# Kernel optimization log

Hardware: AMD Instinct MI355X
Metric: run time of the kernel (lower is better)

The kernel has to match this reference:

```python
import jax, jax.numpy as jnp
import numpy as np

DIM = 768
HEADS = 12
HEAD_DIM = DIM // HEADS
SCALE = HEAD_DIM ** -0.5


def setup_inputs() -> dict:
    key = jax.random.key(0)
    k1, k2, k3, k4, k5 = jax.random.split(key, 5)
    B, N = 4, 2048
    x = jax.random.normal(k1, (B, N, DIM), dtype=jnp.float32)
    # qkv Linear: weight [3*dim, dim], bias [3*dim]
    w_qkv = jax.random.normal(k2, (3 * DIM, DIM), dtype=jnp.float32) * (DIM ** -0.5)
    b_qkv = jax.random.normal(k3, (3 * DIM,), dtype=jnp.float32) * 0.01
    # proj Linear: weight [dim, dim], bias [dim]
    w_proj = jax.random.normal(k4, (DIM, DIM), dtype=jnp.float32) * (DIM ** -0.5)
    b_proj = jax.random.normal(k5, (DIM,), dtype=jnp.float32) * 0.01
    return {"x": x, "w_qkv": w_qkv, "b_qkv": b_qkv, "w_proj": w_proj, "b_proj": b_proj}


def reference(x, w_qkv, b_qkv, w_proj, b_proj):
    B, N, C = x.shape
    qkv = (jnp.einsum('bnc,oc->bno', x, w_qkv) + b_qkv)
    qkv = qkv.reshape(B, N, 3, HEADS, HEAD_DIM).transpose(2, 0, 3, 1, 4)
    q, k, v = qkv[0], qkv[1], qkv[2]
    attn = jnp.einsum('bhqd,bhkd->bhqk', q, k) * SCALE
    attn = jax.nn.softmax(attn, axis=-1)
    out = jnp.einsum('bhqk,bhkd->bhqd', attn, v)  # [B, H, N, Dh]
    out = out.transpose(0, 2, 1, 3).reshape(B, N, C)
    # dropout is identity in eval mode
    return jnp.einsum('bnc,oc->bno', out, w_proj) + b_proj
```

## Files before the change

### kernel.cpp

```cpp
#include <hip/hip_runtime.h>
#include <hip/hip_bf16.h>

using bf16 = __hip_bfloat16;
typedef __bf16 bf16x8 __attribute__((ext_vector_type(8)));
typedef short short4v __attribute__((ext_vector_type(4)));
typedef short short8v __attribute__((ext_vector_type(8)));
typedef float float4v __attribute__((ext_vector_type(4)));

#define DIM   768
#define NH    12
#define HD    64
#define SEQ   2048
#define BATCH 4
#define TOK   (BATCH * SEQ)
#define SCALE_QL2E 0.18033688011112042f

#define NX  (TOK * DIM)
#define NWQ (3 * DIM * DIM)
#define NWP (DIM * DIM)

__device__ __forceinline__ short f2bf(float f) {
  union { bf16 h; short s; } u;
  u.h = __float2bfloat16(f);
  return u.s;
}

union frag8 { short4v h[2]; short8v s; bf16x8 b; };

__device__ __forceinline__ void async_copy16(const bf16* g, short* l) {
  __builtin_amdgcn_global_load_lds(
      (const __attribute__((address_space(1))) unsigned int*)g,
      (__attribute__((address_space(3))) unsigned int*)l, 16, 0, 0);
}
__device__ __forceinline__ void async_copy4(const bf16* g, short* l) {
  __builtin_amdgcn_global_load_lds(
      (const __attribute__((address_space(1))) unsigned int*)g,
      (__attribute__((address_space(3))) unsigned int*)l, 4, 0, 0);
}

__global__ void __launch_bounds__(256)
cvt3(const float* __restrict__ a, bf16* __restrict__ oa, long na,
     const float* __restrict__ b, bf16* __restrict__ ob, long nb,
     const float* __restrict__ c, bf16* __restrict__ oc, long nc) {
  const long i = ((long)blockIdx.x * 256 + threadIdx.x) * 8;
  const float* src; bf16* dst; long off;
  if (i < na)                { src = a; dst = oa; off = i; }
  else if (i < na + nb)      { src = b; dst = ob; off = i - na; }
  else if (i < na + nb + nc) { src = c; dst = oc; off = i - na - nb; }
  else return;
  const float4v x0 = *(const float4v*)(src + off);
  const float4v x1 = *(const float4v*)(src + off + 4);
  short8v r;
  r[0] = f2bf(x0[0]); r[1] = f2bf(x0[1]); r[2] = f2bf(x0[2]); r[3] = f2bf(x0[3]);
  r[4] = f2bf(x1[0]); r[5] = f2bf(x1[1]); r[6] = f2bf(x1[2]); r[7] = f2bf(x1[3]);
  *(short8v*)(dst + off) = r;
}

__device__ __forceinline__ void gemm_mainloop(const bf16* __restrict__ A,
                                              const bf16* __restrict__ B,
                                              short* As, short* Bs,
                                              float4v acc[4][4]) {
  const int t = threadIdx.x;
  const int w = t >> 6, l = t & 63, lr = l & 15, q = l >> 4;
  const int wr = ((w >> 1) << 6), wc = ((w & 1) << 6);

  const bf16* Ag = A + (t >> 2) * DIM + (t & 3) * 8;
  const bf16* Bg = B + (t >> 2) * DIM + (t & 3) * 8;

  for (int k0 = 0; k0 < DIM; k0 += 32) {
    __syncthreads();
    async_copy16(Ag,            &As[t * 8]);
    async_copy16(Ag + 64 * DIM, &As[2048 + t * 8]);
    async_copy16(Bg,            &Bs[t * 8]);
    async_copy16(Bg + 64 * DIM, &Bs[2048 + t * 8]);
    Ag += 32; Bg += 32;
    __syncthreads();

    bf16x8 af[4], bfv[4];
#pragma unroll
    for (int i = 0; i < 4; ++i)
      af[i] = *(const bf16x8*)&As[(wr + i * 16 + lr) * 32 + q * 8];
#pragma unroll
    for (int j = 0; j < 4; ++j)
      bfv[j] = *(const bf16x8*)&Bs[(wc + j * 16 + lr) * 32 + q * 8];
#pragma unroll
    for (int i = 0; i < 4; ++i)
#pragma unroll
      for (int j = 0; j < 4; ++j)
        acc[i][j] = __builtin_amdgcn_mfma_f32_16x16x32_bf16(af[i], bfv[j],
                                                            acc[i][j], 0, 0, 0);
  }
}

#define VW0 asm volatile("s_waitcnt vmcnt(0)" ::: "memory")
#define BARRIER __builtin_amdgcn_s_barrier()
#define LGKM0 asm volatile("s_waitcnt lgkmcnt(0)" ::: "memory")
#define NOSTG (void)0
#define NOVW  (void)0

#define STGP(s, p)                                                            \
  async_copy16(pa + (p) * 32,             &As[s][t * 8]);                     \
  async_copy16(pa + 64 * DIM + (p) * 32,  &As[s][2048 + t * 8]);              \
  async_copy16(pb + (p) * 32,             &Bs[s][t * 8]);                     \
  async_copy16(pb + 64 * DIM + (p) * 32,  &Bs[s][2048 + t * 8]);              \
  async_copy16(pb + 128 * DIM + (p) * 32, &Bs[s][4096 + t * 8]);              \
  async_copy16(pb + 192 * DIM + (p) * 32, &Bs[s][6144 + t * 8]);              \
  async_copy4 (pb3 + (p) * 32,            &Bs[s][8192 + t * 2]);              \
  async_copy4 (pb3 + 16 * DIM + (p) * 32, &Bs[s][8704 + t * 2])

#define PHASE(CUR, STG_, VW_) {                                               \
  bf16x8 af[4], bfv[9];                                                       \
  _Pragma("unroll") for (int mf_ = 0; mf_ < 4; ++mf_)                         \
    af[mf_] = *(const bf16x8*)&As[CUR][mf_ * 512 + arow];                     \
  _Pragma("unroll") for (int nf_ = 0; nf_ < 9; ++nf_)                         \
    bfv[nf_] = *(const bf16x8*)&Bs[CUR][nf_ * 512 + brow];                    \
  STG_; BARRIER; LGKM0;                                                       \
  __builtin_amdgcn_s_setprio(1);                                              \
  _Pragma("unroll") for (int mf_ = 0; mf_ < 4; ++mf_)                         \
  _Pragma("unroll") for (int nf_ = 0; nf_ < 9; ++nf_)                         \
    acc[mf_][nf_] = __builtin_amdgcn_mfma_f32_16x16x32_bf16(                  \
        af[mf_], bfv[nf_], acc[mf_][nf_], 0, 0, 0);                           \
  __builtin_amdgcn_s_setprio(0); VW_; BARRIER; }

__global__ void __launch_bounds__(256, 2)
gemm_qkv(const bf16* __restrict__ X, const bf16* __restrict__ W,
         const float* __restrict__ bias,
         bf16* __restrict__ qb, bf16* __restrict__ kb, bf16* __restrict__ vb) {
  __shared__ short As[2][128 * 32];
  __shared__ short Bs[2][288 * 32];
  const int t = threadIdx.x;
  const int w = t >> 6, l = t & 63, lr = l & 15, q = l >> 4;
  const int wm = w >> 1, wn = w & 1;

  const int orig = blockIdx.x;
  const int swz = (orig & 7) * 64 + (orig >> 3);
  const int tm = swz >> 3, tn = swz & 7;
  const int row0 = tm * 128, col0 = tn * 288;

  const int sr = t >> 2;
  const int scol = (((t & 3) << 3) ^ (((sr >> 1) & 3) << 3));
  const bf16* pa  = X + (size_t)(row0 + sr) * DIM + scol;
  const bf16* pb  = W + (size_t)(col0 + sr) * DIM + scol;
  const int r3 = t >> 4;
  const int c3 = ((t & 15) << 1) ^ (((r3 >> 1) & 3) << 3);
  const bf16* pb3 = W + (size_t)(col0 + 256 + r3) * DIM + c3;

  const int acol = ((q << 3) ^ (((lr >> 1) & 3) << 3));
  const int arow = (wm * 64 + lr) * 32 + acol;
  const int brow = (wn * 144 + lr) * 32 + acol;

  float4v acc[4][9] = {};

  STGP(0, 0);
  VW0; BARRIER;

#pragma unroll 1
  for (int k = 0; k < 22; k += 2) {
    PHASE(0, STGP(1, k + 1), VW0)
    PHASE(1, STGP(0, k + 2), VW0)
  }
  PHASE(0, STGP(1, 23), VW0)
  PHASE(1, NOSTG,       NOVW)

#pragma unroll
  for (int nf = 0; nf < 9; ++nf) {
    const int gn = col0 + wn * 144 + nf * 16 + lr;
    const int which = gn / DIM;
    const int cc = gn - which * DIM;
    const int hh = cc >> 6, dd = cc & 63;
    const float bv = bias[gn];
#pragma unroll
    for (int mf = 0; mf < 4; ++mf) {
      const int gm0 = row0 + wm * 64 + mf * 16 + (q << 2);
      const int b = gm0 >> 11, n0 = gm0 & 2047;
      if (which == 2) {
        short4v pv;
#pragma unroll
        for (int r = 0; r < 4; ++r) pv[r] = f2bf(acc[mf][nf][r] + bv);
        *(short4v*)&vb[((size_t)(b * NH + hh) * HD + dd) * SEQ + n0] = pv;
      } else {
        bf16* dst = (which == 0) ? qb : kb;
        const float sc = (which == 0) ? SCALE_QL2E : 1.0f;
#pragma unroll
        for (int r = 0; r < 4; ++r)
          dst[((size_t)(b * NH + hh) * SEQ + n0 + r) * HD + dd] =
              __float2bfloat16((acc[mf][nf][r] + bv) * sc);
      }
    }
  }
}

__global__ void __launch_bounds__(256, 3)
flash_attn(const bf16* __restrict__ Qp, const bf16* __restrict__ Kp,
           const bf16* __restrict__ Vtp, bf16* __restrict__ Op) {
  const int bh = blockIdx.y, qt = blockIdx.x;
  const int t = threadIdx.x, w = t >> 6, l = t & 63, lr = l & 15, q = l >> 4;
  __shared__ short Ks[2][64 * 68];
  __shared__ short Vt[2][64 * 66];

  const bf16* Qb = Qp  + (size_t)(bh * SEQ + qt * 128) * HD;
  const bf16* Kb = Kp  + (size_t)bh * SEQ * HD;
  const bf16* Vb = Vtp + (size_t)bh * HD * SEQ;

  const int tr3 = t >> 3, td8 = (t & 7) * 8;

#pragma unroll
  for (int i = 0; i < 4; ++i) {
    const int row = i * 32 + tr3;
    *(short8v*)&Ks[row >> 6][(row & 63) * 68 + td8] =
        *(const short8v*)(Qb + (size_t)row * HD + td8);
  }
  __syncthreads();
  bf16x8 qf[2][2];
#pragma unroll
  for (int it = 0; it < 2; ++it)
#pragma unroll
    for (int kq = 0; kq < 2; ++kq) {
      const int row = w * 32 + it * 16 + lr;
      qf[it][kq] = *(const bf16x8*)&Ks[row >> 6][(row & 63) * 68 + kq * 32 + q * 8];
    }
  __syncthreads();

  short8v kr[2], vr[2];
#pragma unroll
  for (int i = 0; i < 2; ++i) {
    kr[i] = *(const short8v*)(Kb + (size_t)(i * 32 + tr3) * HD + td8);
    vr[i] = *(const short8v*)(Vb + (size_t)(i * 32 + tr3) * SEQ + td8);
  }

  frag8 ones;
#pragma unroll
  for (int r = 0; r < 8; ++r) ones.s[r] = (short)0x3F80;

  float4v o[2][4] = {};
  float4v lacc[2] = {};

  for (int kt = 0; kt < 32; ++kt) {
    const int cur = kt & 1;
#pragma unroll
    for (int i = 0; i < 2; ++i) {
      *(short8v*)&Ks[cur][(i * 32 + tr3) * 68 + td8] = kr[i];
      *(short8v*)&Vt[cur][(i * 32 + tr3) * 66 + td8] = vr[i];
    }
    if (kt < 31) {
      const int k1 = (kt + 1) * 64;
#pragma unroll
      for (int i = 0; i < 2; ++i) {
        kr[i] = *(const short8v*)(Kb + (size_t)(k1 + i * 32 + tr3) * HD + td8);
        vr[i] = *(const short8v*)(Vb + (size_t)(i * 32 + tr3) * SEQ + k1 + td8);
      }
    }
    __syncthreads();

    float4v s[4][2] = {};
    __builtin_amdgcn_s_setprio(1);
#pragma unroll
    for (int jn = 0; jn < 4; ++jn) {
      bf16x8 kf[2];
#pragma unroll
      for (int kq = 0; kq < 2; ++kq)
        kf[kq] = *(const bf16x8*)&Ks[cur][(jn * 16 + lr) * 68 + kq * 32 + q * 8];
#pragma unroll
      for (int it = 0; it < 2; ++it)
#pragma unroll
        for (int kq = 0; kq < 2; ++kq)
          s[jn][it] = __builtin_amdgcn_mfma_f32_16x16x32_bf16(kf[kq], qf[it][kq],
                                                              s[jn][it], 0, 0, 0);
    }
    __builtin_amdgcn_s_setprio(0);

    frag8 pf[2][2];
#pragma unroll
    for (int it = 0; it < 2; ++it)
#pragma unroll
      for (int c4 = 0; c4 < 2; ++c4)
#pragma unroll
        for (int r = 0; r < 4; ++r) {
          pf[c4][it].s[r]     = f2bf(__builtin_amdgcn_exp2f(s[2 * c4][it][r]));
          pf[c4][it].s[4 + r] = f2bf(__builtin_amdgcn_exp2f(s[2 * c4 + 1][it][r]));
        }

    __builtin_amdgcn_s_setprio(1);
#pragma unroll
    for (int c4 = 0; c4 < 2; ++c4) {
#pragma unroll
      for (int dj = 0; dj < 4; ++dj) {
        frag8 vf;
        vf.h[0] = *(const short4v*)&Vt[cur][(dj * 16 + lr) * 66 + c4 * 32 + (q << 2)];
        vf.h[1] = *(const short4v*)&Vt[cur][(dj * 16 + lr) * 66 + c4 * 32 + 16 + (q << 2)];
#pragma unroll
        for (int it = 0; it < 2; ++it)
          o[it][dj] = __builtin_amdgcn_mfma_f32_16x16x32_bf16(pf[c4][it].b, vf.b,
                                                              o[it][dj], 0, 0, 0);
      }
#pragma unroll
      for (int it = 0; it < 2; ++it)
        lacc[it] = __builtin_amdgcn_mfma_f32_16x16x32_bf16(pf[c4][it].b, ones.b,
                                                           lacc[it], 0, 0, 0);
    }
    __builtin_amdgcn_s_setprio(0);
  }

  const int b = bh / NH, h = bh - b * NH;
#pragma unroll
  for (int it = 0; it < 2; ++it)
#pragma unroll
    for (int r = 0; r < 4; ++r) {
      const float linv = 1.0f / lacc[it][r];
      const int grow = b * SEQ + qt * 128 + w * 32 + it * 16 + (q << 2) + r;
      bf16* orow = Op + (size_t)grow * DIM + h * HD;
#pragma unroll
      for (int dj = 0; dj < 4; ++dj)
        orow[dj * 16 + lr] = __float2bfloat16(o[it][dj][r] * linv);
    }
}

__global__ void __launch_bounds__(256)
gemm_proj(const bf16* __restrict__ A, const bf16* __restrict__ W,
          const float* __restrict__ bias, float* __restrict__ out) {
  __shared__ short As[128 * 32];
  __shared__ short Bs[128 * 32];
  const int t = threadIdx.x;
  const int w = t >> 6, l = t & 63, lr = l & 15, q = l >> 4;
  const int wr = ((w >> 1) << 6), wc = ((w & 1) << 6);
  const int row0 = blockIdx.y * 128, col0 = blockIdx.x * 128;

  float4v acc[4][4] = {};
  gemm_mainloop(A + row0 * DIM, W + col0 * DIM, As, Bs, acc);

#pragma unroll
  for (int j = 0; j < 4; ++j) {
    const int gn = col0 + wc + j * 16 + lr;
    const float bv = bias[gn];
#pragma unroll
    for (int i = 0; i < 4; ++i) {
#pragma unroll
      for (int r = 0; r < 4; ++r) {
        const int gm = row0 + wr + i * 16 + (q << 2) + r;
        out[(size_t)gm * DIM + gn] = acc[i][j][r] + bv;
      }
    }
  }
}

extern "C" void kernel_launch(void* const* d_in, const int* in_sizes, int n_in,
                              void* d_out, int out_size, void* d_ws, size_t ws_size,
                              hipStream_t stream) {
  const float* x      = (const float*)d_in[0];
  const float* w_qkv  = (const float*)d_in[1];
  const float* b_qkv  = (const float*)d_in[2];
  const float* w_proj = (const float*)d_in[3];
  const float* b_proj = (const float*)d_in[4];
  float* out = (float*)d_out;

  const size_t perbuf = (size_t)BATCH * NH * SEQ * HD;
  bf16* qb  = (bf16*)d_ws;
  bf16* kb  = qb + perbuf;
  bf16* vb  = kb + perbuf;
  bf16* ao  = vb + perbuf;
  bf16* xb  = ao + perbuf;
  bf16* wqb = xb + (size_t)NX;
  bf16* wpb = wqb + (size_t)NWQ;

  const int cvt_blocks = (NX + NWQ + NWP) / 8 / 256;
  cvt3<<<cvt_blocks, 256, 0, stream>>>(x, xb, NX, w_qkv, wqb, NWQ, w_proj, wpb, NWP);
  gemm_qkv <<<dim3(512), 256, 0, stream>>>(xb, wqb, b_qkv, qb, kb, vb);
  flash_attn<<<dim3(SEQ / 128, BATCH * NH), 256, 0, stream>>>(qb, kb, vb, ao);
  gemm_proj <<<dim3(DIM / 128, TOK / 128),  256, 0, stream>>>(ao, wpb, b_proj, out);
}
```

Baseline: 205.8 us.

## Enlarge QKV GEMM tile to 256x288 with 8 waves and split-quadrant pipelined staging

Rewrites the QKV projection GEMM to use 512-thread blocks, each computing a 256x288 output tile with a K-step of 64. Operand tiles are split into four shared-memory sub-buffers, and global-to-LDS copies for the next tile are interleaved between the four quadrant MFMA sub-phases, with partial vmcnt waits so loads stay in flight. The larger tile increases operand reuse and halves the grid to 256 blocks, at the cost of much more LDS per block, more barriers, and fewer blocks, which may hurt occupancy and the tail on the device.

```diff
diff --git a/kernel.cpp b/kernel.cpp
--- a/kernel.cpp
+++ b/kernel.cpp
@@ -92,86 +92,128 @@
   }
 }
 
+#define VW8 asm volatile("s_waitcnt vmcnt(8)" ::: "memory")
 #define VW0 asm volatile("s_waitcnt vmcnt(0)" ::: "memory")
 #define BARRIER __builtin_amdgcn_s_barrier()
 #define LGKM0 asm volatile("s_waitcnt lgkmcnt(0)" ::: "memory")
 #define NOSTG (void)0
 #define NOVW  (void)0
 
-#define STGP(s, p)                                                            \
-  async_copy16(pa + (p) * 32,             &As[s][t * 8]);                     \
-  async_copy16(pa + 64 * DIM + (p) * 32,  &As[s][2048 + t * 8]);              \
-  async_copy16(pb + (p) * 32,             &Bs[s][t * 8]);                     \
-  async_copy16(pb + 64 * DIM + (p) * 32,  &Bs[s][2048 + t * 8]);              \
-  async_copy16(pb + 128 * DIM + (p) * 32, &Bs[s][4096 + t * 8]);              \
-  async_copy16(pb + 192 * DIM + (p) * 32, &Bs[s][6144 + t * 8]);              \
-  async_copy4 (pb3 + (p) * 32,            &Bs[s][8192 + t * 2]);              \
-  async_copy4 (pb3 + 16 * DIM + (p) * 32, &Bs[s][8704 + t * 2])
-
-#define PHASE(CUR, STG_, VW_) {                                               \
-  bf16x8 af[4], bfv[9];                                                       \
-  _Pragma("unroll") for (int mf_ = 0; mf_ < 4; ++mf_)                         \
-    af[mf_] = *(const bf16x8*)&As[CUR][mf_ * 512 + arow];                     \
-  _Pragma("unroll") for (int nf_ = 0; nf_ < 9; ++nf_)                         \
-    bfv[nf_] = *(const bf16x8*)&Bs[CUR][nf_ * 512 + brow];                    \
-  STG_; BARRIER; LGKM0;                                                       \
+#define STG_A0(c, k) { async_copy16(pa    + (k),      &As0[c][t * 8]);        \
+                       async_copy16(pa    + (k) + 32, &As0[c][4096 + t * 8]); }
+#define STG_A1(c, k) { async_copy16(pa128 + (k),      &As1[c][t * 8]);        \
+                       async_copy16(pa128 + (k) + 32, &As1[c][4096 + t * 8]); }
+#define STG_B0(c, k) { async_copy16(pw0   + (k),      &Bs0[c][t * 8]);        \
+                       async_copy16(pw0   + (k) + 32, &Bs0[c][4096 + t * 8]); }
+#define STG_B1(c, k) { async_copy16(pw128 + (k),      &Bs1[c][t * 8]);        \
+                       async_copy4 (pw256 + (k),      &Bs1[c][4096 + t * 2]); \
+                       async_copy16(pw128 + (k) + 32, &Bs1[c][5120 + t * 8]); \
+                       async_copy4 (pw256 + (k) + 32, &Bs1[c][9216 + t * 2]); }
+
+#define KTILE(C, ST1, ST2, ST3, ST4, VW_) {                                   \
+  bf16x8 a0[2][2], a1[2][2], b0[4][2], b1[5][2];                              \
+  _Pragma("unroll") for (int m_ = 0; m_ < 2; ++m_) {                          \
+    a0[m_][0] = *(const bf16x8*)&As0[C][m_ * 2048 + arow];                    \
+    a0[m_][1] = *(const bf16x8*)&As0[C][4096 + m_ * 2048 + arow]; }           \
+  _Pragma("unroll") for (int n_ = 0; n_ < 4; ++n_) {                          \
+    b0[n_][0] = *(const bf16x8*)&Bs0[C][n_ * 1024 + brow];                    \
+    b0[n_][1] = *(const bf16x8*)&Bs0[C][4096 + n_ * 1024 + brow]; }           \
+  ST1; BARRIER; LGKM0;                                                        \
   __builtin_amdgcn_s_setprio(1);                                              \
-  _Pragma("unroll") for (int mf_ = 0; mf_ < 4; ++mf_)                         \
-  _Pragma("unroll") for (int nf_ = 0; nf_ < 9; ++nf_)                         \
-    acc[mf_][nf_] = __builtin_amdgcn_mfma_f32_16x16x32_bf16(                  \
-        af[mf_], bfv[nf_], acc[mf_][nf_], 0, 0, 0);                           \
+  _Pragma("unroll") for (int m_ = 0; m_ < 2; ++m_)                            \
+  _Pragma("unroll") for (int n_ = 0; n_ < 4; ++n_)                            \
+  _Pragma("unroll") for (int p_ = 0; p_ < 2; ++p_)                            \
+    acc[m_][n_] = __builtin_amdgcn_mfma_f32_16x16x32_bf16(                    \
+        a0[m_][p_], b0[n_][p_], acc[m_][n_], 0, 0, 0);                        \
+  __builtin_amdgcn_s_setprio(0); BARRIER;                                     \
+  _Pragma("unroll") for (int m_ = 0; m_ < 2; ++m_) {                          \
+    a1[m_][0] = *(const bf16x8*)&As1[C][m_ * 2048 + arow];                    \
+    a1[m_][1] = *(const bf16x8*)&As1[C][4096 + m_ * 2048 + arow]; }           \
+  ST2; BARRIER; LGKM0;                                                        \
+  __builtin_amdgcn_s_setprio(1);                                              \
+  _Pragma("unroll") for (int m_ = 0; m_ < 2; ++m_)                            \
+  _Pragma("unroll") for (int n_ = 0; n_ < 4; ++n_)                            \
+  _Pragma("unroll") for (int p_ = 0; p_ < 2; ++p_)                            \
+    acc[2 + m_][n_] = __builtin_amdgcn_mfma_f32_16x16x32_bf16(                \
+        a1[m_][p_], b0[n_][p_], acc[2 + m_][n_], 0, 0, 0);                    \
+  __builtin_amdgcn_s_setprio(0); BARRIER;                                     \
+  _Pragma("unroll") for (int n_ = 0; n_ < 5; ++n_) {                          \
+    b1[n_][0] = *(const bf16x8*)&Bs1[C][n_ * 1024 + brow];                    \
+    b1[n_][1] = *(const bf16x8*)&Bs1[C][5120 + n_ * 1024 + brow]; }           \
+  ST3; BARRIER; LGKM0;                                                        \
+  __builtin_amdgcn_s_setprio(1);                                              \
+  _Pragma("unroll") for (int m_ = 0; m_ < 2; ++m_)                            \
+  _Pragma("unroll") for (int n_ = 0; n_ < 5; ++n_)                            \
+  _Pragma("unroll") for (int p_ = 0; p_ < 2; ++p_)                            \
+    acc[m_][4 + n_] = __builtin_amdgcn_mfma_f32_16x16x32_bf16(                \
+        a0[m_][p_], b1[n_][p_], acc[m_][4 + n_], 0, 0, 0);                    \
+  __builtin_amdgcn_s_setprio(0); BARRIER;                                     \
+  ST4; BARRIER;                                                               \
+  __builtin_amdgcn_s_setprio(1);                                              \
+  _Pragma("unroll") for (int m_ = 0; m_ < 2; ++m_)                            \
+  _Pragma("unroll") for (int n_ = 0; n_ < 5; ++n_)                            \
+  _Pragma("unroll") for (int p_ = 0; p_ < 2; ++p_)                            \
+    acc[2 + m_][4 + n_] = __builtin_amdgcn_mfma_f32_16x16x32_bf16(            \
+        a1[m_][p_], b1[n_][p_], acc[2 + m_][4 + n_], 0, 0, 0);                \
   __builtin_amdgcn_s_setprio(0); VW_; BARRIER; }
 
-__global__ void __launch_bounds__(256, 2)
+__global__ void __launch_bounds__(512, 2)
 gemm_qkv(const bf16* __restrict__ X, const bf16* __restrict__ W,
          const float* __restrict__ bias,
          bf16* __restrict__ qb, bf16* __restrict__ kb, bf16* __restrict__ vb) {
-  __shared__ short As[2][128 * 32];
-  __shared__ short Bs[2][288 * 32];
+  __shared__ short As0[2][8192];
+  __shared__ short As1[2][8192];
+  __shared__ short Bs0[2][8192];
+  __shared__ short Bs1[2][10240];
   const int t = threadIdx.x;
   const int w = t >> 6, l = t & 63, lr = l & 15, q = l >> 4;
   const int wm = w >> 1, wn = w & 1;
 
   const int orig = blockIdx.x;
-  const int swz = (orig & 7) * 64 + (orig >> 3);
+  const int swz = (orig & 7) * 32 + (orig >> 3);
   const int tm = swz >> 3, tn = swz & 7;
-  const int row0 = tm * 128, col0 = tn * 288;
+  const int row0 = tm * 256, col0 = tn * 288;
 
   const int sr = t >> 2;
   const int scol = (((t & 3) << 3) ^ (((sr >> 1) & 3) << 3));
-  const bf16* pa  = X + (size_t)(row0 + sr) * DIM + scol;
-  const bf16* pb  = W + (size_t)(col0 + sr) * DIM + scol;
-  const int r3 = t >> 4;
-  const int c3 = ((t & 15) << 1) ^ (((r3 >> 1) & 3) << 3);
-  const bf16* pb3 = W + (size_t)(col0 + 256 + r3) * DIM + c3;
+  const bf16* pa    = X + (size_t)(row0 + sr) * DIM + scol;
+  const bf16* pa128 = X + (size_t)(row0 + 128 + sr) * DIM + scol;
+  const bf16* pw0   = W + (size_t)(col0 + sr) * DIM + scol;
+  const bf16* pw128 = W + (size_t)(col0 + 128 + sr) * DIM + scol;
+  const int r4 = t >> 4;
+  const int c4s = ((t & 15) << 1) ^ (((r4 >> 1) & 3) << 3);
+  const bf16* pw256 = W + (size_t)(col0 + 256 + r4) * DIM + c4s;
 
   const int acol = ((q << 3) ^ (((lr >> 1) & 3) << 3));
-  const int arow = (wm * 64 + lr) * 32 + acol;
-  const int brow = (wn * 144 + lr) * 32 + acol;
+  const int arow = (wm * 16 + lr) * 32 + acol;
+  const int brow = (wn * 16 + lr) * 32 + acol;
 
   float4v acc[4][9] = {};
 
-  STGP(0, 0);
-  VW0; BARRIER;
+  STG_A0(0, 0); STG_B0(0, 0); STG_B1(0, 0); STG_A1(0, 0);
+  STG_A0(1, 64); STG_B0(1, 64); STG_B1(1, 64);
+  VW8; BARRIER;
 
 #pragma unroll 1
-  for (int k = 0; k < 22; k += 2) {
-    PHASE(0, STGP(1, k + 1), VW0)
-    PHASE(1, STGP(0, k + 2), VW0)
-  }
-  PHASE(0, STGP(1, 23), VW0)
-  PHASE(1, NOSTG,       NOVW)
+  for (int i = 0; i < 5; ++i) {
+    KTILE(0, STG_A1(1, 64),  STG_A0(0, 128), STG_B0(0, 128), STG_B1(0, 128), VW8)
+    KTILE(1, STG_A1(0, 128), STG_A0(1, 192), STG_B0(1, 192), STG_B1(1, 192), VW8)
+    pa += 128; pa128 += 128; pw0 += 128; pw128 += 128; pw256 += 128;
+  }
+  KTILE(0, STG_A1(1, 64), NOSTG, NOSTG, NOSTG, VW0)
+  KTILE(1, NOSTG, NOSTG, NOSTG, NOSTG, NOVW)
 
 #pragma unroll
   for (int nf = 0; nf < 9; ++nf) {
-    const int gn = col0 + wn * 144 + nf * 16 + lr;
+    const int bcol = (nf < 4) ? nf * 32 : 128 + (nf - 4) * 32;
+    const int gn = col0 + bcol + wn * 16 + lr;
     const int which = gn / DIM;
     const int cc = gn - which * DIM;
     const int hh = cc >> 6, dd = cc & 63;
     const float bv = bias[gn];
 #pragma unroll
     for (int mf = 0; mf < 4; ++mf) {
-      const int gm0 = row0 + wm * 64 + mf * 16 + (q << 2);
+      const int gm0 = row0 + mf * 64 + wm * 16 + (q << 2);
       const int b = gm0 >> 11, n0 = gm0 & 2047;
       if (which == 2) {
         short4v pv;
@@ -364,7 +406,7 @@
 
   const int cvt_blocks = (NX + NWQ + NWP) / 8 / 256;
   cvt3<<<cvt_blocks, 256, 0, stream>>>(x, xb, NX, w_qkv, wqb, NWQ, w_proj, wpb, NWP);
-  gemm_qkv <<<dim3(512), 256, 0, stream>>>(xb, wqb, b_qkv, qb, kb, vb);
+  gemm_qkv <<<dim3(256), 512, 0, stream>>>(xb, wqb, b_qkv, qb, kb, vb);
   flash_attn<<<dim3(SEQ / 128, BATCH * NH), 256, 0, stream>>>(qb, kb, vb, ao);
   gemm_proj <<<dim3(DIM / 128, TOK / 128),  256, 0, stream>>>(ao, wpb, b_proj, out);
 }
```

After: 209.3 us. About the same (+1.7%).

## Use async global-to-LDS loads with 4-stage ring buffer in flash attention

Applied to the files above, without the earlier changes.

Replaces the register-staged K/V double buffer in the attention kernel with direct global_load_lds copies into a 4-slot LDS ring. Loads are issued two tiles ahead and gated by vmcnt waits and a single barrier per tile, instead of a register round-trip plus __syncthreads. Padding-based bank-conflict avoidance is replaced by an XOR swizzle, and Q fragments are now read straight from global memory. LDS use grows to 64 KB, so occupancy is lowered from 3 to 2 blocks per CU, which may reduce latency hiding.

```diff
diff --git a/kernel.cpp b/kernel.cpp
--- a/kernel.cpp
+++ b/kernel.cpp
@@ -37,6 +37,14 @@
       (const __attribute__((address_space(1))) unsigned int*)g,
       (__attribute__((address_space(3))) unsigned int*)l, 4, 0, 0);
 }
+
+#define BARRIER __builtin_amdgcn_s_barrier()
+#define LGKM0 asm volatile("s_waitcnt lgkmcnt(0)" ::: "memory")
+#define VW0 asm volatile("s_waitcnt vmcnt(0)" ::: "memory")
+#define VW4 asm volatile("s_waitcnt vmcnt(4)" ::: "memory")
+#define VW8 asm volatile("s_waitcnt vmcnt(8)" ::: "memory")
+#define NOSTG (void)0
+#define NOVW  (void)0
 
 __global__ void __launch_bounds__(256)
 cvt3(const float* __restrict__ a, bf16* __restrict__ oa, long na,
@@ -92,12 +100,6 @@
   }
 }
 
-#define VW0 asm volatile("s_waitcnt vmcnt(0)" ::: "memory")
-#define BARRIER __builtin_amdgcn_s_barrier()
-#define LGKM0 asm volatile("s_waitcnt lgkmcnt(0)" ::: "memory")
-#define NOSTG (void)0
-#define NOVW  (void)0
-
 #define STGP(s, p)                                                            \
   async_copy16(pa + (p) * 32,             &As[s][t * 8]);                     \
   async_copy16(pa + 64 * DIM + (p) * 32,  &As[s][2048 + t * 8]);              \
@@ -190,43 +192,35 @@
   }
 }
 
-__global__ void __launch_bounds__(256, 3)
+#define STG_KV(bb, k1)                                                        \
+  async_copy16(Kb + (size_t)((k1) + drow) * HD + skey,       &KV[bb][t * 8]); \
+  async_copy16(Kb + (size_t)((k1) + 32 + drow) * HD + skey,  &KV[bb][2048 + t * 8]); \
+  async_copy16(Vb + (size_t)drow * SEQ + (k1) + skey,        &KV[bb][4096 + t * 8]); \
+  async_copy16(Vb + (size_t)(32 + drow) * SEQ + (k1) + skey, &KV[bb][6144 + t * 8])
+
+__global__ void __launch_bounds__(256, 2)
 flash_attn(const bf16* __restrict__ Qp, const bf16* __restrict__ Kp,
            const bf16* __restrict__ Vtp, bf16* __restrict__ Op) {
   const int bh = blockIdx.y, qt = blockIdx.x;
   const int t = threadIdx.x, w = t >> 6, l = t & 63, lr = l & 15, q = l >> 4;
-  __shared__ short Ks[2][64 * 68];
-  __shared__ short Vt[2][64 * 66];
+  __shared__ short KV[4][8192];
 
   const bf16* Qb = Qp  + (size_t)(bh * SEQ + qt * 128) * HD;
   const bf16* Kb = Kp  + (size_t)bh * SEQ * HD;
   const bf16* Vb = Vtp + (size_t)bh * HD * SEQ;
 
-  const int tr3 = t >> 3, td8 = (t & 7) * 8;
-
-#pragma unroll
-  for (int i = 0; i < 4; ++i) {
-    const int row = i * 32 + tr3;
-    *(short8v*)&Ks[row >> 6][(row & 63) * 68 + td8] =
-        *(const short8v*)(Qb + (size_t)row * HD + td8);
-  }
-  __syncthreads();
+  const int drow = t >> 3;
+  const int skey = (((t & 7) ^ drow) & 7) * 8;
+
   bf16x8 qf[2][2];
 #pragma unroll
   for (int it = 0; it < 2; ++it)
 #pragma unroll
-    for (int kq = 0; kq < 2; ++kq) {
-      const int row = w * 32 + it * 16 + lr;
-      qf[it][kq] = *(const bf16x8*)&Ks[row >> 6][(row & 63) * 68 + kq * 32 + q * 8];
-    }
-  __syncthreads();
-
-  short8v kr[2], vr[2];
-#pragma unroll
-  for (int i = 0; i < 2; ++i) {
-    kr[i] = *(const short8v*)(Kb + (size_t)(i * 32 + tr3) * HD + td8);
-    vr[i] = *(const short8v*)(Vb + (size_t)(i * 32 + tr3) * SEQ + td8);
-  }
+    for (int kq = 0; kq < 2; ++kq)
+      qf[it][kq] = *(const bf16x8*)(Qb + (size_t)(w * 32 + it * 16 + lr) * HD +
+                                    kq * 32 + q * 8);
+
+  const int key8 = (lr & 7) << 3;
 
   frag8 ones;
 #pragma unroll
@@ -235,22 +229,14 @@
   float4v o[2][4] = {};
   float4v lacc[2] = {};
 
+  STG_KV(0, 0);
+  STG_KV(1, 64);
+
   for (int kt = 0; kt < 32; ++kt) {
-    const int cur = kt & 1;
-#pragma unroll
-    for (int i = 0; i < 2; ++i) {
-      *(short8v*)&Ks[cur][(i * 32 + tr3) * 68 + td8] = kr[i];
-      *(short8v*)&Vt[cur][(i * 32 + tr3) * 66 + td8] = vr[i];
-    }
-    if (kt < 31) {
-      const int k1 = (kt + 1) * 64;
-#pragma unroll
-      for (int i = 0; i < 2; ++i) {
-        kr[i] = *(const short8v*)(Kb + (size_t)(k1 + i * 32 + tr3) * HD + td8);
-        vr[i] = *(const short8v*)(Vb + (size_t)(i * 32 + tr3) * SEQ + k1 + td8);
-      }
-    }
-    __syncthreads();
+    if (kt < 30) { STG_KV((kt + 2) & 3, (kt + 2) * 64); }
+    if (kt < 30) { VW8; } else if (kt == 30) { VW4; } else { VW0; }
+    BARRIER;
+    const short* Bf = KV[kt & 3];
 
     float4v s[4][2] = {};
     __builtin_amdgcn_s_setprio(1);
@@ -259,7 +245,8 @@
       bf16x8 kf[2];
 #pragma unroll
       for (int kq = 0; kq < 2; ++kq)
-        kf[kq] = *(const bf16x8*)&Ks[cur][(jn * 16 + lr) * 68 + kq * 32 + q * 8];
+        kf[kq] = *(const bf16x8*)&Bf[(jn * 16 + lr) * 64 +
+                                     (((kq * 32) + (q << 3)) ^ key8)];
 #pragma unroll
       for (int it = 0; it < 2; ++it)
 #pragma unroll
@@ -286,8 +273,10 @@
 #pragma unroll
       for (int dj = 0; dj < 4; ++dj) {
         frag8 vf;
-        vf.h[0] = *(const short4v*)&Vt[cur][(dj * 16 + lr) * 66 + c4 * 32 + (q << 2)];
-        vf.h[1] = *(const short4v*)&Vt[cur][(dj * 16 + lr) * 66 + c4 * 32 + 16 + (q << 2)];
+        vf.h[0] = *(const short4v*)&Bf[4096 + (dj * 16 + lr) * 64 +
+                                       ((c4 * 32 + (q << 2)) ^ key8)];
+        vf.h[1] = *(const short4v*)&Bf[4096 + (dj * 16 + lr) * 64 +
+                                       ((c4 * 32 + 16 + (q << 2)) ^ key8)];
 #pragma unroll
         for (int it = 0; it < 2; ++it)
           o[it][dj] = __builtin_amdgcn_mfma_f32_16x16x32_bf16(pf[c4][it].b, vf.b,
```

After: 206.6 us. No clear change (+0.4%).
